# Optimization experiments

Hardware: AMD Instinct MI355X
Metric: run time of the kernel (lower is better)

The kernel has to match this reference:

```python
import jax, jax.numpy as jnp
import numpy as np

D, H, HD, L, F, V, R, C = 512, 8, 64, 12, 2048, 2048, 1024, 64
B, T, M = 8, 1024, 128


def posenc(t, d):
    pos = jnp.arange(t, dtype=jnp.float32)[:, None]
    div = jnp.exp(jnp.arange(0, d, 2, dtype=jnp.float32) * (-np.log(10000.0) / d))
    pe = jnp.zeros((t, d), jnp.float32)
    pe = pe.at[:, 0::2].set(jnp.sin(pos * div))
    pe = pe.at[:, 1::2].set(jnp.cos(pos * div))
    return pe


def setup_inputs():
    key = jax.random.key(0)
    ks = iter(jax.random.split(key, 32))
    s = 0.02
    x = jax.random.randint(next(ks), (B, T), 1, V)  # avoid padding_idx=0 rows
    chord_positions = jax.random.randint(next(ks), (B, M), 0, T)
    n = lambda shape: jax.random.normal(next(ks), shape, jnp.float32) * s
    emb = n((V, D)).at[0].set(0.0)  # padding_idx row zeroed
    return {
        'x': x, 'chord_positions': chord_positions, 'emb': emb,
        'rel_emb': n((L, 2 * R + 1, HD)),
        'Wq': n((L, D, D)), 'bq': jnp.zeros((L, D)),
        'Wk': n((L, D, D)), 'bk': jnp.zeros((L, D)),
        'Wv': n((L, D, D)), 'bv': jnp.zeros((L, D)),
        'Wo': n((L, D, D)), 'bo': jnp.zeros((L, D)),
        'ln1_s': jnp.ones((L, D)), 'ln1_b': jnp.zeros((L, D)),
        'W1': n((L, D, F)), 'b1': jnp.zeros((L, F)),
        'W2': n((L, F, D)), 'b2': jnp.zeros((L, D)),
        'ln2_s': jnp.ones((L, D)), 'ln2_b': jnp.zeros((L, D)),
        'Wout': n((D, V)), 'bout': jnp.zeros((V,)),
        'Wc': n((D, C)), 'bc': jnp.zeros((C,)),
    }


def _ln(z, s, b):
    mu = jnp.mean(z, -1, keepdims=True)
    var = jnp.var(z, -1, keepdims=True)
    return (z - mu) * jax.lax.rsqrt(var + 1e-5) * s + b


def _forward(x, chord_positions, emb, rel_emb, Wq, bq, Wk, bk, Wv, bv, Wo, bo,
             ln1_s, ln1_b, W1, b1, W2, b2, ln2_s, ln2_b, Wout, bout, Wc, bc):
    Bx, Tx = x.shape
    h = emb[x] * jnp.sqrt(jnp.float32(D)) + posenc(Tx, D)[None]
    pad = (x == 0)  # key padding mask
    causal = jnp.triu(jnp.ones((Tx, Tx), bool), 1)
    mask = causal[None, None] | pad[:, None, None, :]  # (B,1|H,T,T)
    rel_idx = jnp.clip(jnp.arange(Tx)[None, :] - jnp.arange(Tx)[:, None], -R, R) + R  # (T,T)
    for i in range(L):
        q = (h @ Wq[i] + bq[i]).reshape(Bx, Tx, H, HD).transpose(0, 2, 1, 3)
        k = (h @ Wk[i] + bk[i]).reshape(Bx, Tx, H, HD).transpose(0, 2, 1, 3)
        v = (h @ Wv[i] + bv[i]).reshape(Bx, Tx, H, HD).transpose(0, 2, 1, 3)
        scores = jnp.einsum('bhqd,bhkd->bhqk', q, k)
        relp = jnp.einsum('bhqd,rd->bhqr', q, rel_emb[i])  # (B,H,T,2R+1)
        scores = scores + jnp.take_along_axis(relp, rel_idx[None, None], axis=-1)
        scores = scores * (1.0 / np.sqrt(HD))
        scores = jnp.where(mask, -1e9, scores)
        a = jax.nn.softmax(scores, axis=-1)
        o = jnp.einsum('bhqk,bhkd->bhqd', a, v).transpose(0, 2, 1, 3).reshape(Bx, Tx, D)
        h = _ln(h + o @ Wo[i] + bo[i], ln1_s[i], ln1_b[i])
        f = jax.nn.relu(h @ W1[i] + b1[i]) @ W2[i] + b2[i]
        h = _ln(h + f, ln2_s[i], ln2_b[i])
    logits = h @ Wout + bout
    safe_pos = jnp.maximum(chord_positions, 0)
    gathered = h[jnp.arange(Bx)[:, None], safe_pos]  # (B,M,D)
    chord_logits = gathered @ Wc + bc
    return logits, chord_logits


def reference(x, chord_positions, emb, rel_emb, Wq, bq, Wk, bk, Wv, bv, Wo, bo,
              ln1_s, ln1_b, W1, b1, W2, b2, ln2_s, ln2_b, Wout, bout, Wc, bc):
    return _forward(x, chord_positions, emb, rel_emb, Wq, bq, Wk, bk, Wv, bv, Wo, bo,
                    ln1_s, ln1_b, W1, b1, W2, b2, ln2_s, ln2_b, Wout, bout, Wc, bc)
```

## Files before the change

kernel.cpp:

```cpp
#include <hip/hip_runtime.h>
#include <hip/hip_bf16.h>
#include <cstddef>

constexpr int B_ = 8, TT = 1024, H_ = 8, HD_ = 64, D_ = 512, F_ = 2048;
constexpr int L_ = 12, R_ = 1024, NR_ = 2049, C_ = 64, M_ = 128, V_ = 2048;
constexpr int BT_ = B_ * TT;

typedef short bf16x8_t __attribute__((ext_vector_type(8)));
typedef float f32x4_t __attribute__((ext_vector_type(4)));
typedef unsigned short ushort_t;

__device__ __forceinline__ float b2f(unsigned int u16) {
  return __uint_as_float(u16 << 16);
}
__device__ __forceinline__ ushort_t f2b(float f) {
  __hip_bfloat16 h = __float2bfloat16(f);
  return *reinterpret_cast<ushort_t*>(&h);
}

__global__ __launch_bounds__(256) void transpose_bf16_b(const float* __restrict__ src,
                                                        ushort_t* __restrict__ dst,
                                                        int K, int N,
                                                        size_t sstride, size_t dstride) {
  __shared__ float t[32][33];
  src += (size_t)blockIdx.z * sstride;
  dst += (size_t)blockIdx.z * dstride;
  int k0 = blockIdx.y * 32, n0 = blockIdx.x * 32;
  int r = threadIdx.x >> 3, c4 = (threadIdx.x & 7) * 4;
  float4 vv = *(const float4*)(src + (size_t)(k0 + r) * N + n0 + c4);
  t[r][c4] = vv.x; t[r][c4 + 1] = vv.y; t[r][c4 + 2] = vv.z; t[r][c4 + 3] = vv.w;
  __syncthreads();
  ushort4 w;
  w.x = f2b(t[c4 + 0][r]); w.y = f2b(t[c4 + 1][r]);
  w.z = f2b(t[c4 + 2][r]); w.w = f2b(t[c4 + 3][r]);
  *(ushort4*)(dst + (size_t)(n0 + r) * K + k0 + c4) = w;
}

__global__ __launch_bounds__(256) void rel_convert(const float* __restrict__ rel,
                                                   ushort_t* __restrict__ rel_bf) {
  size_t idx = ((size_t)blockIdx.x * 256 + threadIdx.x) * 4;
  const size_t total = (size_t)L_ * NR_ * HD_;
  if (idx >= total) return;
  float4 f = *(const float4*)(rel + idx);
  ushort4 w;
  w.x = f2b(f.x); w.y = f2b(f.y); w.z = f2b(f.z); w.w = f2b(f.w);
  *(ushort4*)(rel_bf + idx) = w;
}

__global__ __launch_bounds__(256) void pack_bias(const float* __restrict__ bq,
                                                 const float* __restrict__ bk,
                                                 const float* __restrict__ bv,
                                                 float* __restrict__ bqkv) {
  int idx = blockIdx.x * 256 + threadIdx.x;
  if (idx >= L_ * 1536) return;
  int l = idx / 1536, c = idx - l * 1536;
  float v;
  if (c < 512) v = bq[l * 512 + c];
  else if (c < 1024) v = bk[l * 512 + (c - 512)];
  else v = bv[l * 512 + (c - 1024)];
  bqkv[idx] = v;
}

__global__ void embed_kernel(const int* __restrict__ x, const float* __restrict__ emb,
                             float* __restrict__ h, ushort_t* __restrict__ h_bf) {
  int bt = blockIdx.x;
  int t = bt & (TT - 1);
  int tok = x[bt];
  const float c = -9.210340371976184f / 512.0f;
  size_t base = (size_t)bt * D_;
  size_t ebase = (size_t)tok * D_;
  for (int d = threadIdx.x; d < D_; d += 256) {
    int i = d >> 1;
    float div = expf((float)(2 * i) * c);
    float arg = (float)t * div;
    float pe = (d & 1) ? cosf(arg) : sinf(arg);
    float vv = emb[ebase + d] * 22.627416997969522f + pe;
    h[base + d] = vv;
    h_bf[base + d] = f2b(vv);
  }
}

template <int OUT_BF16, int RELU>
__global__ __launch_bounds__(256) void gemm_mfma(const ushort_t* __restrict__ A,
                                                 const ushort_t* __restrict__ Bt,
                                                 const float* __restrict__ bias,
                                                 void* __restrict__ Cout,
                                                 int Mm, int N, int K) {
  __shared__ ushort_t As[128 * 32];
  __shared__ ushort_t Bs[128 * 32];
  int tid = threadIdx.x;
  int m0 = blockIdx.y * 128, n0 = blockIdx.x * 128;
  int lane = tid & 63, wid = tid >> 6;
  int wr = wid >> 1, wc = wid & 1;

  f32x4_t acc[4][4];
#pragma unroll
  for (int mi = 0; mi < 4; ++mi)
#pragma unroll
    for (int ni = 0; ni < 4; ++ni) acc[mi][ni] = (f32x4_t){0.f, 0.f, 0.f, 0.f};

  int c0 = tid, c1 = tid + 256;
  int ar0 = c0 >> 2, ap0 = c0 & 3, akg0 = ap0 ^ ((ar0 >> 1) & 3);
  int ar1 = c1 >> 2, ap1 = c1 & 3, akg1 = ap1 ^ ((ar1 >> 1) & 3);
  const ushort_t* Arow0 = A + (size_t)(m0 + ar0) * K + akg0 * 8;
  const ushort_t* Arow1 = A + (size_t)(m0 + ar1) * K + akg1 * 8;
  const ushort_t* Brow0 = Bt + (size_t)(n0 + ar0) * K + akg0 * 8;
  const ushort_t* Brow1 = Bt + (size_t)(n0 + ar1) * K + akg1 * 8;

  uint4 ra0 = *(const uint4*)(Arow0);
  uint4 ra1 = *(const uint4*)(Arow1);
  uint4 rb0 = *(const uint4*)(Brow0);
  uint4 rb1 = *(const uint4*)(Brow1);

  int NT = K >> 5;
  int kg = lane >> 4, rl = lane & 15;
  for (int kt = 0; kt < NT; ++kt) {
    __syncthreads();
    *(uint4*)&As[ar0 * 32 + ap0 * 8] = ra0;
    *(uint4*)&As[ar1 * 32 + ap1 * 8] = ra1;
    *(uint4*)&Bs[ar0 * 32 + ap0 * 8] = rb0;
    *(uint4*)&Bs[ar1 * 32 + ap1 * 8] = rb1;
    __syncthreads();
    if (kt + 1 < NT) {
      int ko = (kt + 1) << 5;
      ra0 = *(const uint4*)(Arow0 + ko);
      ra1 = *(const uint4*)(Arow1 + ko);
      rb0 = *(const uint4*)(Brow0 + ko);
      rb1 = *(const uint4*)(Brow1 + ko);
    }
    bf16x8_t fa[4], fb[4];
#pragma unroll
    for (int mi = 0; mi < 4; ++mi) {
      int r = wr * 64 + mi * 16 + rl;
      fa[mi] = *(bf16x8_t*)&As[r * 32 + ((kg ^ ((r >> 1) & 3)) << 3)];
    }
#pragma unroll
    for (int ni = 0; ni < 4; ++ni) {
      int r = wc * 64 + ni * 16 + rl;
      fb[ni] = *(bf16x8_t*)&Bs[r * 32 + ((kg ^ ((r >> 1) & 3)) << 3)];
    }
#pragma unroll
    for (int mi = 0; mi < 4; ++mi)
#pragma unroll
      for (int ni = 0; ni < 4; ++ni)
        acc[mi][ni] = __builtin_amdgcn_mfma_f32_16x16x32_bf16(fa[mi], fb[ni], acc[mi][ni], 0, 0, 0);
  }

  int rg = lane >> 4;
#pragma unroll
  for (int ni = 0; ni < 4; ++ni) {
    int col = n0 + wc * 64 + ni * 16 + rl;
    float bv = bias[col];
#pragma unroll
    for (int mi = 0; mi < 4; ++mi) {
      int row0 = m0 + wr * 64 + mi * 16 + rg * 4;
#pragma unroll
      for (int r = 0; r < 4; ++r) {
        float vv = acc[mi][ni][r] + bv;
        if (RELU) vv = fmaxf(vv, 0.0f);
        if (OUT_BF16)
          ((ushort_t*)Cout)[(size_t)(row0 + r) * N + col] = f2b(vv);
        else
          ((float*)Cout)[(size_t)(row0 + r) * N + col] = vv;
      }
    }
  }
}

template <int RELU>
__global__ __launch_bounds__(256) void gemm_bias(const float* __restrict__ A,
                                                 const float* __restrict__ W,
                                                 const float* __restrict__ bias,
                                                 float* __restrict__ Cm,
                                                 int Mm, int N, int K) {
  __shared__ float As[64][17];
  __shared__ float Bs[16][65];
  int tid = threadIdx.x;
  int tx = tid & 15, ty = tid >> 4;
  int row0 = blockIdx.y * 64, col0 = blockIdx.x * 64;
  float acc[4][4] = {};
  int ra = tid >> 4, ca = tid & 15;
  int rb = tid >> 6, cb = tid & 63;
  for (int k0 = 0; k0 < K; k0 += 16) {
    for (int rr = ra; rr < 64; rr += 16)
      As[rr][ca] = A[(size_t)(row0 + rr) * K + k0 + ca];
    for (int rr = rb; rr < 16; rr += 4)
      Bs[rr][cb] = W[(size_t)(k0 + rr) * N + col0 + cb];
    __syncthreads();
#pragma unroll
    for (int kk = 0; kk < 16; ++kk) {
      float a[4], bb[4];
#pragma unroll
      for (int i = 0; i < 4; ++i) a[i] = As[ty * 4 + i][kk];
#pragma unroll
      for (int j = 0; j < 4; ++j) bb[j] = Bs[kk][tx * 4 + j];
#pragma unroll
      for (int i = 0; i < 4; ++i)
#pragma unroll
        for (int j = 0; j < 4; ++j) acc[i][j] += a[i] * bb[j];
    }
    __syncthreads();
  }
#pragma unroll
  for (int i = 0; i < 4; ++i) {
#pragma unroll
    for (int j = 0; j < 4; ++j) {
      float vv = acc[i][j] + bias[col0 + tx * 4 + j];
      if (RELU) vv = fmaxf(vv, 0.0f);
      Cm[(size_t)(row0 + ty * 4 + i) * N + col0 + tx * 4 + j] = vv;
    }
  }
}

__global__ __launch_bounds__(256) void attn_mfma(const ushort_t* __restrict__ qkv,
                                                 const ushort_t* __restrict__ rel_bf,
                                                 ushort_t* __restrict__ o) {
  __shared__ ushort_t QPs[64 * 64];
  __shared__ ushort_t Ks[64 * 64];
  __shared__ ushort_t Vs[64 * 64];
  __shared__ ushort_t Rl[128 * 64];

  int blk = blockIdx.x;
  int u = ((blk & 15) + 5 * ((blk >> 8) & 3)) & 15;
  int qt = (u & 1) ? ((u - 1) >> 1) : (15 - (u >> 1));
  int bh = blk >> 4;
  int hh = bh & 7, b = bh >> 3;
  int t0 = qt << 6;
  int tid = threadIdx.x;
  int lane = tid & 63, w = tid >> 6;
  int lo = lane & 15, hi = lane >> 4;

  const ushort_t* qg = qkv + ((size_t)(b * TT + t0)) * 1536 + hh * 64;
  const ushort_t* kg = qkv + ((size_t)b * TT) * 1536 + 512 + hh * 64;
  const ushort_t* vg = qkv + ((size_t)b * TT) * 1536 + 1024 + hh * 64;
  const ushort_t* relb = rel_bf + (size_t)(961 - t0) * 64;

  int row_a = tid >> 3, gg_a = tid & 7;
  int row_b = row_a + 32;

  for (int idx = tid; idx < 512; idx += 256) {
    int row = idx >> 3, gg = idx & 7;
    uint4 uu = *(const uint4*)(qg + (size_t)row * 1536 + gg * 8);
    unsigned int uw[4] = {uu.x, uu.y, uu.z, uu.w};
    unsigned int ow[4];
#pragma unroll
    for (int j = 0; j < 4; ++j) {
      float f0 = b2f(uw[j] & 0xffffu) * 0.125f;
      float f1 = b2f(uw[j] >> 16) * 0.125f;
      ow[j] = (unsigned int)f2b(f0) | ((unsigned int)f2b(f1) << 16);
    }
    *(uint4*)&QPs[row * 64 + ((gg ^ (row & 7)) << 3)] = make_uint4(ow[0], ow[1], ow[2], ow[3]);
  }
  __syncthreads();

  bf16x8_t faq0 = *(bf16x8_t*)&QPs[(16 * w + lo) * 64 + ((hi ^ (lo & 7)) << 3)];
  bf16x8_t faq1 = *(bf16x8_t*)&QPs[(16 * w + lo) * 64 + (((hi + 4) ^ (lo & 7)) << 3)];

  uint4 pk0 = *(const uint4*)(kg + (size_t)row_a * 1536 + gg_a * 8);
  uint4 pk1 = *(const uint4*)(kg + (size_t)row_b * 1536 + gg_a * 8);
  uint4 pv0 = *(const uint4*)(vg + (size_t)row_a * 1536 + gg_a * 8);
  uint4 pv1 = *(const uint4*)(vg + (size_t)row_b * 1536 + gg_a * 8);
  uint4 pr0 = *(const uint4*)(relb + (size_t)row_a * 64 + gg_a * 8);
  uint4 pr1 = *(const uint4*)(relb + (size_t)(row_a + 32) * 64 + gg_a * 8);
  uint4 pr2 = *(const uint4*)(relb + (size_t)(row_a + 64) * 64 + gg_a * 8);
  uint4 pr3 = *(const uint4*)(relb + (size_t)(row_a + 96) * 64 + gg_a * 8);

  f32x4_t acc_o[4];
#pragma unroll
  for (int nd = 0; nd < 4; ++nd) acc_o[nd] = (f32x4_t){0.f, 0.f, 0.f, 0.f};
  float mrow[4] = {-1e30f, -1e30f, -1e30f, -1e30f};
  float lrow[4] = {0.f, 0.f, 0.f, 0.f};

  int vsb = (int)(size_t)(const void*)Vs;
  int tb0 = vsb + ((2 * hi + 0) * 4) * 128 + lo * 8;
  int tb1 = vsb + ((2 * hi + 1) * 4) * 128 + lo * 8;
  int tb2 = vsb + ((2 * hi + 8) * 4) * 128 + lo * 8;
  int tb3 = vsb + ((2 * hi + 9) * 4) * 128 + lo * 8;

  int nkt = (t0 >> 6) + 1;
  for (int kt = 0; kt < nkt; ++kt) {
    __syncthreads();
    *(uint4*)&Ks[row_a * 64 + ((gg_a ^ (row_a & 7)) << 3)] = pk0;
    *(uint4*)&Ks[row_b * 64 + ((gg_a ^ (row_b & 7)) << 3)] = pk1;
    *(uint4*)&Vs[((row_a >> 2) * 4 + (gg_a >> 1)) * 64 + (row_a & 3) * 16 + (gg_a & 1) * 8] = pv0;
    *(uint4*)&Vs[((row_b >> 2) * 4 + (gg_a >> 1)) * 64 + (row_b & 3) * 16 + (gg_a & 1) * 8] = pv1;
    if (kt == 0) {
      int u0 = row_a;
      *(uint4*)&Rl[u0 * 64 + ((gg_a ^ (u0 & 7)) << 3)] = pr0;
      int u1 = row_a + 32;
      *(uint4*)&Rl[u1 * 64 + ((gg_a ^ (u1 & 7)) << 3)] = pr1;
      int u2 = row_a + 64;
      *(uint4*)&Rl[u2 * 64 + ((gg_a ^ (u2 & 7)) << 3)] = pr2;
      int u3 = row_a + 96;
      *(uint4*)&Rl[u3 * 64 + ((gg_a ^ (u3 & 7)) << 3)] = pr3;
    } else {
      int ur0 = 64 + row_a, ph0 = (ur0 + (kt << 6)) & 127;
      *(uint4*)&Rl[ph0 * 64 + ((gg_a ^ (ur0 & 7)) << 3)] = pr0;
      int ur1 = 64 + row_b, ph1 = (ur1 + (kt << 6)) & 127;
      *(uint4*)&Rl[ph1 * 64 + ((gg_a ^ (ur1 & 7)) << 3)] = pr1;
    }
    __syncthreads();
    if (kt + 1 < nkt) {
      size_t ko = (size_t)((kt + 1) << 6);
      pk0 = *(const uint4*)(kg + (ko + row_a) * 1536 + gg_a * 8);
      pk1 = *(const uint4*)(kg + (ko + row_b) * 1536 + gg_a * 8);
      pv0 = *(const uint4*)(vg + (ko + row_a) * 1536 + gg_a * 8);
      pv1 = *(const uint4*)(vg + (ko + row_b) * 1536 + gg_a * 8);
      pr0 = *(const uint4*)(relb + (ko + 64 + row_a) * 64 + gg_a * 8);
      pr1 = *(const uint4*)(relb + (ko + 64 + row_b) * 64 + gg_a * 8);
    }

    f32x4_t acc_s[4], acc_r[5];
#pragma unroll
    for (int nc = 0; nc < 4; ++nc) acc_s[nc] = (f32x4_t){0.f, 0.f, 0.f, 0.f};
#pragma unroll
    for (int pt = 0; pt < 5; ++pt) acc_r[pt] = (f32x4_t){0.f, 0.f, 0.f, 0.f};

    __builtin_amdgcn_s_setprio(1);
#pragma unroll
    for (int nc = 0; nc < 4; ++nc) {
      int row = 16 * nc + lo;
      bf16x8_t fb0 = *(bf16x8_t*)&Ks[row * 64 + ((hi ^ (lo & 7)) << 3)];
      bf16x8_t fb1 = *(bf16x8_t*)&Ks[row * 64 + (((hi + 4) ^ (lo & 7)) << 3)];
      acc_s[nc] = __builtin_amdgcn_mfma_f32_16x16x32_bf16(faq0, fb0, acc_s[nc], 0, 0, 0);
      acc_s[nc] = __builtin_amdgcn_mfma_f32_16x16x32_bf16(faq1, fb1, acc_s[nc], 0, 0, 0);
    }
#pragma unroll
    for (int pt = 0; pt < 5; ++pt) {
      int r = 16 * (3 - w + pt) + lo;
      int phys = (r + (kt << 6)) & 127;
      bf16x8_t fb0 = *(bf16x8_t*)&Rl[phys * 64 + ((hi ^ (lo & 7)) << 3)];
      bf16x8_t fb1 = *(bf16x8_t*)&Rl[phys * 64 + (((hi + 4) ^ (lo & 7)) << 3)];
      acc_r[pt] = __builtin_amdgcn_mfma_f32_16x16x32_bf16(faq0, fb0, acc_r[pt], 0, 0, 0);
      acc_r[pt] = __builtin_amdgcn_mfma_f32_16x16x32_bf16(faq1, fb1, acc_r[pt], 0, 0, 0);
    }
    __builtin_amdgcn_s_setprio(0);

    bool islast = (kt == nkt - 1);
#pragma unroll
    for (int g = 0; g < 4; ++g) {
      int rl = 4 * hi + g;
      int dd = lo + 15 - rl;
      int src = (lane & 48) | (dd & 15);
      bool carry = (dd & 16) != 0;
      float sh0 = __shfl(acc_r[0][g], src);
      float sh1 = __shfl(acc_r[1][g], src);
      float sh2 = __shfl(acc_r[2][g], src);
      float sh3 = __shfl(acc_r[3][g], src);
      float sh4 = __shfl(acc_r[4][g], src);
      float s0 = acc_s[0][g] + (carry ? sh1 : sh0);
      float s1 = acc_s[1][g] + (carry ? sh2 : sh1);
      float s2 = acc_s[2][g] + (carry ? sh3 : sh2);
      float s3 = acc_s[3][g] + (carry ? sh4 : sh3);
      if (islast) {
        int rw = 16 * w + rl;
        if (lo > rw) s0 = -1e30f;
        if (16 + lo > rw) s1 = -1e30f;
        if (32 + lo > rw) s2 = -1e30f;
        if (48 + lo > rw) s3 = -1e30f;
      }
      float mx = fmaxf(fmaxf(s0, s1), fmaxf(s2, s3));
      mx = fmaxf(mx, __shfl_xor(mx, 1));
      mx = fmaxf(mx, __shfl_xor(mx, 2));
      mx = fmaxf(mx, __shfl_xor(mx, 4));
      mx = fmaxf(mx, __shfl_xor(mx, 8));
      float mnew = fmaxf(mrow[g], mx);
      float scale = __expf(mrow[g] - mnew);
      mrow[g] = mnew;
      float p0 = __expf(s0 - mnew);
      float p1 = __expf(s1 - mnew);
      float p2 = __expf(s2 - mnew);
      float p3 = __expf(s3 - mnew);
      float ls = p0 + p1 + p2 + p3;
      ls += __shfl_xor(ls, 1);
      ls += __shfl_xor(ls, 2);
      ls += __shfl_xor(ls, 4);
      ls += __shfl_xor(ls, 8);
      lrow[g] = lrow[g] * scale + ls;
      acc_o[0][g] *= scale; acc_o[1][g] *= scale;
      acc_o[2][g] *= scale; acc_o[3][g] *= scale;
      ushort_t* pr = &QPs[(16 * w + rl) * 64];
      int rsw = rl & 7, l3 = lo >> 3, l7 = lo & 7;
      pr[(((0 + l3) ^ rsw) << 3) + l7] = f2b(p0);
      pr[(((2 + l3) ^ rsw) << 3) + l7] = f2b(p1);
      pr[(((4 + l3) ^ rsw) << 3) + l7] = f2b(p2);
      pr[(((6 + l3) ^ rsw) << 3) + l7] = f2b(p3);
    }

    bf16x8_t pa0 = *(bf16x8_t*)&QPs[(16 * w + lo) * 64 + ((hi ^ (lo & 7)) << 3)];
    bf16x8_t pa1 = *(bf16x8_t*)&QPs[(16 * w + lo) * 64 + (((hi + 4) ^ (lo & 7)) << 3)];
    unsigned long long tr0[4], tr1[4], tr2[4], tr3[4];
#pragma unroll
    for (int nd = 0; nd < 4; ++nd) {
      asm volatile("ds_read_b64_tr_b16 %0, %1" : "=v"(tr0[nd]) : "v"(tb0 + nd * 128));
      asm volatile("ds_read_b64_tr_b16 %0, %1" : "=v"(tr1[nd]) : "v"(tb1 + nd * 128));
      asm volatile("ds_read_b64_tr_b16 %0, %1" : "=v"(tr2[nd]) : "v"(tb2 + nd * 128));
      asm volatile("ds_read_b64_tr_b16 %0, %1" : "=v"(tr3[nd]) : "v"(tb3 + nd * 128));
    }
    asm volatile("s_waitcnt lgkmcnt(0)" ::: "memory");
    __builtin_amdgcn_sched_barrier(0);
    __builtin_amdgcn_s_setprio(1);
#pragma unroll
    for (int nd = 0; nd < 4; ++nd) {
      union { unsigned long long u[2]; bf16x8_t v; } cv0, cv1;
      cv0.u[0] = tr0[nd]; cv0.u[1] = tr1[nd];
      cv1.u[0] = tr2[nd]; cv1.u[1] = tr3[nd];
      acc_o[nd] = __builtin_amdgcn_mfma_f32_16x16x32_bf16(pa0, cv0.v, acc_o[nd], 0, 0, 0);
      acc_o[nd] = __builtin_amdgcn_mfma_f32_16x16x32_bf16(pa1, cv1.v, acc_o[nd], 0, 0, 0);
    }
    __builtin_amdgcn_s_setprio(0);
  }

  ushort_t* og = o + ((size_t)(b * TT + t0 + 16 * w)) * D_ + hh * HD_;
#pragma unroll
  for (int g = 0; g < 4; ++g) {
    int rl = 4 * hi + g;
    float inv = 1.0f / lrow[g];
#pragma unroll
    for (int nd = 0; nd < 4; ++nd)
      og[(size_t)rl * D_ + 16 * nd + lo] = f2b(acc_o[nd][g] * inv);
  }
}

__global__ __launch_bounds__(256) void ln_res_kernel(float* __restrict__ h,
                                                     const float* __restrict__ y,
                                                     const float* __restrict__ s,
                                                     const float* __restrict__ bvec,
                                                     ushort_t* __restrict__ h_bf) {
  int row = blockIdx.x;
  int tid = threadIdx.x;
  size_t base = (size_t)row * D_;
  float z0 = h[base + tid] + y[base + tid];
  float z1 = h[base + tid + 256] + y[base + tid + 256];
  __shared__ float r1[256], r2[256];
  r1[tid] = z0 + z1;
  r2[tid] = z0 * z0 + z1 * z1;
  __syncthreads();
  for (int off = 128; off > 0; off >>= 1) {
    if (tid < off) {
      r1[tid] += r1[tid + off];
      r2[tid] += r2[tid + off];
    }
    __syncthreads();
  }
  float mu = r1[0] * (1.0f / 512.0f);
  float var = r2[0] * (1.0f / 512.0f) - mu * mu;
  float rs = rsqrtf(var + 1e-5f);
  float o0 = (z0 - mu) * rs * s[tid] + bvec[tid];
  float o1 = (z1 - mu) * rs * s[tid + 256] + bvec[tid + 256];
  h[base + tid] = o0;
  h[base + tid + 256] = o1;
  h_bf[base + tid] = f2b(o0);
  h_bf[base + tid + 256] = f2b(o1);
}

__global__ void gather_kernel(const float* __restrict__ h, const int* __restrict__ pos,
                              float* __restrict__ g) {
  int row = blockIdx.x;
  int b = row >> 7;
  int p = pos[row];
  if (p < 0) p = 0;
  size_t src = ((size_t)(b * TT + p)) * D_;
  size_t dst = (size_t)row * D_;
  for (int d = threadIdx.x; d < D_; d += 256) g[dst + d] = h[src + d];
}

extern "C" void kernel_launch(void* const* d_in, const int* in_sizes, int n_in,
                              void* d_out, int out_size, void* d_ws, size_t ws_size,
                              hipStream_t stream) {
  const int* x = (const int*)d_in[0];
  const int* cpos = (const int*)d_in[1];
  const float* emb = (const float*)d_in[2];
  const float* rel = (const float*)d_in[3];
  const float* Wq = (const float*)d_in[4];
  const float* bq = (const float*)d_in[5];
  const float* Wk = (const float*)d_in[6];
  const float* bk = (const float*)d_in[7];
  const float* Wv = (const float*)d_in[8];
  const float* bv = (const float*)d_in[9];
  const float* Wo = (const float*)d_in[10];
  const float* bo = (const float*)d_in[11];
  const float* ln1s = (const float*)d_in[12];
  const float* ln1b = (const float*)d_in[13];
  const float* W1 = (const float*)d_in[14];
  const float* b1 = (const float*)d_in[15];
  const float* W2 = (const float*)d_in[16];
  const float* b2 = (const float*)d_in[17];
  const float* ln2s = (const float*)d_in[18];
  const float* ln2b = (const float*)d_in[19];
  const float* Wout = (const float*)d_in[20];
  const float* bout = (const float*)d_in[21];
  const float* Wc = (const float*)d_in[22];
  const float* bc = (const float*)d_in[23];

  const size_t SZ = (size_t)BT_ * D_;
  const size_t WPROJ = (size_t)D_ * D_;
  const size_t WFFN = (size_t)D_ * F_;

  float* h = (float*)d_ws;
  float* y = h + SZ;
  ushort_t* h_bf = (ushort_t*)(y + SZ);
  ushort_t* qkv_bf = h_bf + SZ;
  ushort_t* o_bf = qkv_bf + (size_t)BT_ * 1536;
  ushort_t* mid_bf = o_bf + SZ;
  ushort_t* wqkvT = mid_bf + (size_t)BT_ * F_;
  ushort_t* woT = wqkvT + (size_t)L_ * 1536 * 512;
  ushort_t* w1T = woT + L_ * WPROJ;
  ushort_t* w2T = w1T + L_ * WFFN;
  ushort_t* woutT = w2T + L_ * WFFN;
  ushort_t* wcT = woutT + (size_t)D_ * V_;
  ushort_t* rel_bf = wcT + (size_t)D_ * C_;
  float* bqkv = (float*)(rel_bf + (size_t)L_ * NR_ * HD_);
  float* gath = bqkv + L_ * 1536;
  float* out = (float*)d_out;

  transpose_bf16_b<<<dim3(16, 16, 12), 256, 0, stream>>>(Wq, wqkvT, 512, 512, WPROJ, (size_t)1536 * 512);
  transpose_bf16_b<<<dim3(16, 16, 12), 256, 0, stream>>>(Wk, wqkvT + (size_t)512 * 512, 512, 512, WPROJ, (size_t)1536 * 512);
  transpose_bf16_b<<<dim3(16, 16, 12), 256, 0, stream>>>(Wv, wqkvT + (size_t)1024 * 512, 512, 512, WPROJ, (size_t)1536 * 512);
  transpose_bf16_b<<<dim3(16, 16, 12), 256, 0, stream>>>(Wo, woT, 512, 512, WPROJ, WPROJ);
  transpose_bf16_b<<<dim3(64, 16, 12), 256, 0, stream>>>(W1, w1T, 512, 2048, WFFN, WFFN);
  transpose_bf16_b<<<dim3(16, 64, 12), 256, 0, stream>>>(W2, w2T, 2048, 512, WFFN, WFFN);
  transpose_bf16_b<<<dim3(64, 16, 1), 256, 0, stream>>>(Wout, woutT, 512, 2048, 0, 0);
  transpose_bf16_b<<<dim3(2, 16, 1), 256, 0, stream>>>(Wc, wcT, 512, 64, 0, 0);
  rel_convert<<<1537, 256, 0, stream>>>(rel, rel_bf);
  pack_bias<<<(L_ * 1536 + 255) / 256, 256, 0, stream>>>(bq, bk, bv, bqkv);

  embed_kernel<<<BT_, 256, 0, stream>>>(x, emb, h, h_bf);

  dim3 gQKV(1536 / 128, BT_ / 128);
  dim3 gProj(D_ / 128, BT_ / 128);
  dim3 gF1(F_ / 128, BT_ / 128);
  dim3 gOut(V_ / 128, BT_ / 128);

  for (int l = 0; l < L_; ++l) {
    gemm_mfma<1, 0><<<gQKV, 256, 0, stream>>>(h_bf, wqkvT + (size_t)l * 1536 * 512,
                                              bqkv + l * 1536, qkv_bf, BT_, 1536, D_);
    attn_mfma<<<B_ * H_ * (TT / 64), 256, 0, stream>>>(qkv_bf, rel_bf + (size_t)l * NR_ * HD_, o_bf);
    gemm_mfma<0, 0><<<gProj, 256, 0, stream>>>(o_bf, woT + l * WPROJ, bo + l * D_, y, BT_, D_, D_);
    ln_res_kernel<<<BT_, 256, 0, stream>>>(h, y, ln1s + l * D_, ln1b + l * D_, h_bf);
    gemm_mfma<1, 1><<<gF1, 256, 0, stream>>>(h_bf, w1T + l * WFFN, b1 + l * F_, mid_bf, BT_, F_, D_);
    gemm_mfma<0, 0><<<gProj, 256, 0, stream>>>(mid_bf, w2T + l * WFFN, b2 + l * D_, y, BT_, D_, F_);
    ln_res_kernel<<<BT_, 256, 0, stream>>>(h, y, ln2s + l * D_, ln2b + l * D_, h_bf);
  }

  gemm_mfma<0, 0><<<gOut, 256, 0, stream>>>(h_bf, woutT, bout, out, BT_, V_, D_);
  gather_kernel<<<B_ * M_, 256, 0, stream>>>(h, cpos, gath);
  gemm_bias<0><<<dim3(1, (B_ * M_) / 64), 256, 0, stream>>>(gath, Wc, bc, out + (size_t)BT_ * V_,
                                                            B_ * M_, C_, D_);
}
```

Baseline: 2.542 ms.

## Double-buffer GEMM tiles via direct global-to-LDS loads and fuse chord gather into MFMA

The main bf16 GEMM now double-buffers its A/B tiles in shared memory and fills them with global_load_lds, which copies straight into LDS without a register round trip and removes one barrier per k-step. The gather and fp32 chord GEMM are replaced by one MFMA kernel that reads the gathered rows of h_bf directly. The LDS layout now relies on the direct-load lane order matching the existing swizzle, which is subtle, and the chord head now uses bf16 inputs, which lowers its precision.

```diff
diff --git a/kernel.cpp b/kernel.cpp
--- a/kernel.cpp
+++ b/kernel.cpp
@@ -16,6 +16,11 @@
 __device__ __forceinline__ ushort_t f2b(float f) {
   __hip_bfloat16 h = __float2bfloat16(f);
   return *reinterpret_cast<ushort_t*>(&h);
+}
+__device__ __forceinline__ void gl_lds16(const ushort_t* g, ushort_t* l) {
+  __builtin_amdgcn_global_load_lds(
+      (const __attribute__((address_space(1))) unsigned int*)g,
+      (__attribute__((address_space(3))) unsigned int*)l, 16, 0, 0);
 }
 
 __global__ __launch_bounds__(256) void transpose_bf16_b(const float* __restrict__ src,
@@ -86,8 +91,8 @@
                                                  const float* __restrict__ bias,
                                                  void* __restrict__ Cout,
                                                  int Mm, int N, int K) {
-  __shared__ ushort_t As[128 * 32];
-  __shared__ ushort_t Bs[128 * 32];
+  __shared__ ushort_t As[2][128 * 32];
+  __shared__ ushort_t Bs[2][128 * 32];
   int tid = threadIdx.x;
   int m0 = blockIdx.y * 128, n0 = blockIdx.x * 128;
   int lane = tid & 63, wid = tid >> 6;
@@ -99,51 +104,48 @@
 #pragma unroll
     for (int ni = 0; ni < 4; ++ni) acc[mi][ni] = (f32x4_t){0.f, 0.f, 0.f, 0.f};
 
-  int c0 = tid, c1 = tid + 256;
-  int ar0 = c0 >> 2, ap0 = c0 & 3, akg0 = ap0 ^ ((ar0 >> 1) & 3);
-  int ar1 = c1 >> 2, ap1 = c1 & 3, akg1 = ap1 ^ ((ar1 >> 1) & 3);
-  const ushort_t* Arow0 = A + (size_t)(m0 + ar0) * K + akg0 * 8;
-  const ushort_t* Arow1 = A + (size_t)(m0 + ar1) * K + akg1 * 8;
-  const ushort_t* Brow0 = Bt + (size_t)(n0 + ar0) * K + akg0 * 8;
-  const ushort_t* Brow1 = Bt + (size_t)(n0 + ar1) * K + akg1 * 8;
-
-  uint4 ra0 = *(const uint4*)(Arow0);
-  uint4 ra1 = *(const uint4*)(Arow1);
-  uint4 rb0 = *(const uint4*)(Brow0);
-  uint4 rb1 = *(const uint4*)(Brow1);
+  int ar0 = tid >> 2, ap0 = tid & 3, akg0 = ap0 ^ ((ar0 >> 1) & 3);
+  int ar1 = ar0 + 64, akg1 = ap0 ^ ((ar1 >> 1) & 3);
+  const ushort_t* sA0 = A + (size_t)(m0 + ar0) * K + akg0 * 8;
+  const ushort_t* sA1 = A + (size_t)(m0 + ar1) * K + akg1 * 8;
+  const ushort_t* sB0 = Bt + (size_t)(n0 + ar0) * K + akg0 * 8;
+  const ushort_t* sB1 = Bt + (size_t)(n0 + ar1) * K + akg1 * 8;
+  int lo8 = tid * 8;
+
+  gl_lds16(sA0, &As[0][lo8]);
+  gl_lds16(sA1, &As[0][lo8 + 2048]);
+  gl_lds16(sB0, &Bs[0][lo8]);
+  gl_lds16(sB1, &Bs[0][lo8 + 2048]);
 
   int NT = K >> 5;
   int kg = lane >> 4, rl = lane & 15;
+  int buf = 0;
   for (int kt = 0; kt < NT; ++kt) {
-    __syncthreads();
-    *(uint4*)&As[ar0 * 32 + ap0 * 8] = ra0;
-    *(uint4*)&As[ar1 * 32 + ap1 * 8] = ra1;
-    *(uint4*)&Bs[ar0 * 32 + ap0 * 8] = rb0;
-    *(uint4*)&Bs[ar1 * 32 + ap1 * 8] = rb1;
     __syncthreads();
     if (kt + 1 < NT) {
       int ko = (kt + 1) << 5;
-      ra0 = *(const uint4*)(Arow0 + ko);
-      ra1 = *(const uint4*)(Arow1 + ko);
-      rb0 = *(const uint4*)(Brow0 + ko);
-      rb1 = *(const uint4*)(Brow1 + ko);
+      gl_lds16(sA0 + ko, &As[buf ^ 1][lo8]);
+      gl_lds16(sA1 + ko, &As[buf ^ 1][lo8 + 2048]);
+      gl_lds16(sB0 + ko, &Bs[buf ^ 1][lo8]);
+      gl_lds16(sB1 + ko, &Bs[buf ^ 1][lo8 + 2048]);
     }
     bf16x8_t fa[4], fb[4];
 #pragma unroll
     for (int mi = 0; mi < 4; ++mi) {
       int r = wr * 64 + mi * 16 + rl;
-      fa[mi] = *(bf16x8_t*)&As[r * 32 + ((kg ^ ((r >> 1) & 3)) << 3)];
+      fa[mi] = *(bf16x8_t*)&As[buf][r * 32 + ((kg ^ ((r >> 1) & 3)) << 3)];
     }
 #pragma unroll
     for (int ni = 0; ni < 4; ++ni) {
       int r = wc * 64 + ni * 16 + rl;
-      fb[ni] = *(bf16x8_t*)&Bs[r * 32 + ((kg ^ ((r >> 1) & 3)) << 3)];
+      fb[ni] = *(bf16x8_t*)&Bs[buf][r * 32 + ((kg ^ ((r >> 1) & 3)) << 3)];
     }
 #pragma unroll
     for (int mi = 0; mi < 4; ++mi)
 #pragma unroll
       for (int ni = 0; ni < 4; ++ni)
         acc[mi][ni] = __builtin_amdgcn_mfma_f32_16x16x32_bf16(fa[mi], fb[ni], acc[mi][ni], 0, 0, 0);
+    buf ^= 1;
   }
 
   int rg = lane >> 4;
@@ -167,47 +169,55 @@
   }
 }
 
-template <int RELU>
-__global__ __launch_bounds__(256) void gemm_bias(const float* __restrict__ A,
-                                                 const float* __restrict__ W,
-                                                 const float* __restrict__ bias,
-                                                 float* __restrict__ Cm,
-                                                 int Mm, int N, int K) {
-  __shared__ float As[64][17];
-  __shared__ float Bs[16][65];
+__global__ __launch_bounds__(256) void chord_mfma(const ushort_t* __restrict__ h_bf,
+                                                  const int* __restrict__ pos,
+                                                  const ushort_t* __restrict__ wcT,
+                                                  const float* __restrict__ bc,
+                                                  float* __restrict__ out) {
+  __shared__ ushort_t As[64 * 32];
+  __shared__ ushort_t Bs[64 * 32];
   int tid = threadIdx.x;
-  int tx = tid & 15, ty = tid >> 4;
-  int row0 = blockIdx.y * 64, col0 = blockIdx.x * 64;
-  float acc[4][4] = {};
-  int ra = tid >> 4, ca = tid & 15;
-  int rb = tid >> 6, cb = tid & 63;
-  for (int k0 = 0; k0 < K; k0 += 16) {
-    for (int rr = ra; rr < 64; rr += 16)
-      As[rr][ca] = A[(size_t)(row0 + rr) * K + k0 + ca];
-    for (int rr = rb; rr < 16; rr += 4)
-      Bs[rr][cb] = W[(size_t)(k0 + rr) * N + col0 + cb];
+  int lane = tid & 63, w = tid >> 6;
+  int rl = lane & 15, kg = lane >> 4;
+  int m0 = blockIdx.x * 64;
+  int ar = tid >> 2, ap = tid & 3, akg = ap ^ ((ar >> 1) & 3);
+  int grow = m0 + ar;
+  int b = grow >> 7;
+  int p = pos[grow];
+  if (p < 0) p = 0;
+  const ushort_t* asrc = h_bf + ((size_t)(b * TT + p)) * D_ + akg * 8;
+  const ushort_t* bsrc = wcT + (size_t)ar * D_ + akg * 8;
+
+  f32x4_t acc[4];
+#pragma unroll
+  for (int ni = 0; ni < 4; ++ni) acc[ni] = (f32x4_t){0.f, 0.f, 0.f, 0.f};
+
+  for (int kt = 0; kt < 16; ++kt) {
+    uint4 va = *(const uint4*)(asrc + kt * 32);
+    uint4 vb = *(const uint4*)(bsrc + kt * 32);
     __syncthreads();
-#pragma unroll
-    for (int kk = 0; kk < 16; ++kk) {
-      float a[4], bb[4];
-#pragma unroll
-      for (int i = 0; i < 4; ++i) a[i] = As[ty * 4 + i][kk];
-#pragma unroll
-      for (int j = 0; j < 4; ++j) bb[j] = Bs[kk][tx * 4 + j];
-#pragma unroll
-      for (int i = 0; i < 4; ++i)
-#pragma unroll
-        for (int j = 0; j < 4; ++j) acc[i][j] += a[i] * bb[j];
-    }
+    *(uint4*)&As[ar * 32 + ap * 8] = va;
+    *(uint4*)&Bs[ar * 32 + ap * 8] = vb;
     __syncthreads();
-  }
-#pragma unroll
-  for (int i = 0; i < 4; ++i) {
-#pragma unroll
-    for (int j = 0; j < 4; ++j) {
-      float vv = acc[i][j] + bias[col0 + tx * 4 + j];
-      if (RELU) vv = fmaxf(vv, 0.0f);
-      Cm[(size_t)(row0 + ty * 4 + i) * N + col0 + tx * 4 + j] = vv;
+    int r = 16 * w + rl;
+    bf16x8_t fa = *(bf16x8_t*)&As[r * 32 + ((kg ^ ((r >> 1) & 3)) << 3)];
+#pragma unroll
+    for (int ni = 0; ni < 4; ++ni) {
+      int rr = ni * 16 + rl;
+      bf16x8_t fb = *(bf16x8_t*)&Bs[rr * 32 + ((kg ^ ((rr >> 1) & 3)) << 3)];
+      acc[ni] = __builtin_amdgcn_mfma_f32_16x16x32_bf16(fa, fb, acc[ni], 0, 0, 0);
+    }
+  }
+
+  int rg = lane >> 4;
+#pragma unroll
+  for (int ni = 0; ni < 4; ++ni) {
+    int col = ni * 16 + rl;
+    float bv = bc[col];
+#pragma unroll
+    for (int r = 0; r < 4; ++r) {
+      int row = m0 + 16 * w + rg * 4 + r;
+      out[(size_t)row * C_ + col] = acc[ni][r] + bv;
     }
   }
 }
@@ -454,17 +464,6 @@
   h_bf[base + tid + 256] = f2b(o1);
 }
 
-__global__ void gather_kernel(const float* __restrict__ h, const int* __restrict__ pos,
-                              float* __restrict__ g) {
-  int row = blockIdx.x;
-  int b = row >> 7;
-  int p = pos[row];
-  if (p < 0) p = 0;
-  size_t src = ((size_t)(b * TT + p)) * D_;
-  size_t dst = (size_t)row * D_;
-  for (int d = threadIdx.x; d < D_; d += 256) g[dst + d] = h[src + d];
-}
-
 extern "C" void kernel_launch(void* const* d_in, const int* in_sizes, int n_in,
                               void* d_out, int out_size, void* d_ws, size_t ws_size,
                               hipStream_t stream) {
@@ -511,7 +510,6 @@
   ushort_t* wcT = woutT + (size_t)D_ * V_;
   ushort_t* rel_bf = wcT + (size_t)D_ * C_;
   float* bqkv = (float*)(rel_bf + (size_t)L_ * NR_ * HD_);
-  float* gath = bqkv + L_ * 1536;
   float* out = (float*)d_out;
 
   transpose_bf16_b<<<dim3(16, 16, 12), 256, 0, stream>>>(Wq, wqkvT, 512, 512, WPROJ, (size_t)1536 * 512);
@@ -544,7 +542,5 @@
   }
 
   gemm_mfma<0, 0><<<gOut, 256, 0, stream>>>(h_bf, woutT, bout, out, BT_, V_, D_);
-  gather_kernel<<<B_ * M_, 256, 0, stream>>>(h, cpos, gath);
-  gemm_bias<0><<<dim3(1, (B_ * M_) / 64), 256, 0, stream>>>(gath, Wc, bc, out + (size_t)BT_ * V_,
-                                                            B_ * M_, C_, D_);
-}
+  chord_mfma<<<(B_ * M_) / 64, 256, 0, stream>>>(h_bf, cpos, wcT, bc, out + (size_t)BT_ * V_);
+}
```

New measurement: 2.585 ms. Within noise of the previous version (+1.7%).
